# Kernel tuning notes

Hardware: AMD Instinct MI355X
Metric: run time of the kernel (lower is better)

Reference implementation:

```python
import jax, jax.numpy as jnp
import numpy as np

I, H, O, K = 64, 512, 3, 6  # input, hidden, output classes, num heads


def setup_inputs() -> dict:
    key = jax.random.key(0)
    ks = jax.random.split(key, 8)
    B, T = 256, 512
    s = 0.05
    return {
        "x": jax.random.normal(ks[0], (B, T, I), dtype=jnp.float32),
        "W_ih": jax.random.normal(ks[1], (4 * H, I), dtype=jnp.float32) * s,
        "W_hh": jax.random.normal(ks[2], (4 * H, H), dtype=jnp.float32) * s,
        "b_ih": jax.random.normal(ks[3], (4 * H,), dtype=jnp.float32) * s,
        "b_hh": jax.random.normal(ks[4], (4 * H,), dtype=jnp.float32) * s,
        "W_heads": jax.random.normal(ks[5], (K, O, H), dtype=jnp.float32) * s,
        "b_heads": jax.random.normal(ks[6], (K, O), dtype=jnp.float32) * s,
    }


def _lstm_last_h(x, W_ih, W_hh, b_ih, b_hh):
    # x: [B, T, I]; returns final hidden state h_T: [B, H]
    B = x.shape[0]
    h0 = jnp.zeros((B, H), dtype=x.dtype)
    c0 = jnp.zeros((B, H), dtype=x.dtype)
    # precompute input projections for all timesteps: [T, B, 4H]
    x_proj = jnp.einsum('bti,gi->tbg', x, W_ih) + b_ih + b_hh

    def step(carry, xp_t):
        h, c = carry
        gates = xp_t + h @ W_hh.T  # [B, 4H]
        i_g, f_g, g_g, o_g = jnp.split(gates, 4, axis=-1)  # PyTorch gate order i,f,g,o
        i_g = jax.nn.sigmoid(i_g)
        f_g = jax.nn.sigmoid(f_g)
        g_g = jnp.tanh(g_g)
        o_g = jax.nn.sigmoid(o_g)
        c = f_g * c + i_g * g_g
        h = o_g * jnp.tanh(c)
        return (h, c), None

    (h_T, _), _ = jax.lax.scan(step, (h0, c0), x_proj)
    return h_T


def reference(x, W_ih, W_hh, b_ih, b_hh, W_heads, b_heads):
    h_T = _lstm_last_h(x, W_ih, W_hh, b_ih, b_hh)  # [B, H]
    # six parallel linear heads on last hidden state -> stacked [6, B, O]
    out = jnp.einsum('koh,bh->kbo', W_heads, h_T) + b_heads[:, None, :]
    return out
```

## Files before the change

### kernel.cpp

```cpp
#include <hip/hip_runtime.h>
#include <hip/hip_bf16.h>
#include <cstdint>

#define TSTEPS 512
#define BATCH  256
#define HID    512
#define INP    64
#define NGRP   16
#define GROWS  16
#define NSL    16
#define NWG    256
#define KTH    16
#define RING   8

typedef __attribute__((ext_vector_type(8))) short short8;
typedef __attribute__((ext_vector_type(4))) float f32x4;
typedef __attribute__((ext_vector_type(2))) float f32x2;
typedef __attribute__((ext_vector_type(2))) unsigned long long ull2;

#define HB_OFF    0
#define HT_OFF    (RING*BATCH*HID*2)
#define FLAGS_OFF (HT_OFF + BATCH*HID*4)
#define FLAGS_SZ  (NGRP*NSL*64)
#define CNT_OFF   (FLAGS_OFF + FLAGS_SZ)
#define ZERO2_SZ  (FLAGS_SZ + 64)

__device__ __forceinline__ unsigned cvtpk(float a, float b) {
    unsigned r;
    asm("v_cvt_pk_bf16_f32 %0, %1, %2" : "=v"(r) : "v"(a), "v"(b));
    return r;
}
__device__ __forceinline__ short8 pack8(float4 a0, float4 a1) {
    uint4 u = { cvtpk(a0.x, a0.y), cvtpk(a0.z, a0.w),
                cvtpk(a1.x, a1.y), cvtpk(a1.z, a1.w) };
    return __builtin_bit_cast(short8, u);
}
__device__ __forceinline__ float sigm(float x)  { return 1.0f/(1.0f + __expf(-x)); }
__device__ __forceinline__ float tanhf_(float x){ return 2.0f/(1.0f + __expf(-2.0f*x)) - 1.0f; }

__global__ void __launch_bounds__(256, 1)
lstm_persist(const float* __restrict__ x,   const float* __restrict__ Wih,
             const float* __restrict__ Whh, const float* __restrict__ bih,
             const float* __restrict__ bhh, const float* __restrict__ Whead,
             const float* __restrict__ bhead, float* __restrict__ out,
             char* __restrict__ ws)
{
    extern __shared__ char lds[];
    const int tid  = threadIdx.x;
    const int lane = tid & 63;
    const int wv   = tid >> 6;
    const int l15  = lane & 15, lq = lane >> 4;

    unsigned short* hb = (unsigned short*)(ws + HB_OFF);
    float* hT  = (float*)(ws + HT_OFF);
    unsigned* flags = (unsigned*)(ws + FLAGS_OFF);
    int* cnt   = (int*)(ws + CNT_OFF);

    int* org = (int*)(lds + 131056);
    if (tid == 0) {
        unsigned xcd;
        asm volatile("s_getreg_b32 %0, hwreg(HW_REG_XCC_ID)" : "=s"(xcd));
        xcd &= 7u;
        int slot = __hip_atomic_fetch_add(&cnt[xcd], 1, __ATOMIC_RELAXED, __HIP_MEMORY_SCOPE_AGENT) & 31;
        org[0] = (int)xcd * 2 + (slot >> 4);
        org[1] = slot & 15;
    }
    __syncthreads();
    const int g  = org[0];
    const int sl = org[1];
    const int hb8 = sl*32 + wv*8;

    short8 whh[KTH][2];
    #pragma unroll
    for (int kt = 0; kt < KTH; ++kt)
        #pragma unroll
        for (int m = 0; m < 2; ++m) {
            int grow = (l15 & 3)*HID + hb8 + m*4 + (l15 >> 2);
            const float4* p = (const float4*)(Whh + (size_t)grow*HID + kt*32 + lq*8);
            whh[kt][m] = pack8(p[0], p[1]);
        }
    short8 wihf[2][2];
    #pragma unroll
    for (int kt = 0; kt < 2; ++kt)
        #pragma unroll
        for (int m = 0; m < 2; ++m) {
            int grow = (l15 & 3)*HID + hb8 + m*4 + (l15 >> 2);
            const float4* p = (const float4*)(Wih + (size_t)grow*INP + kt*32 + lq*8);
            wihf[kt][m] = pack8(p[0], p[1]);
        }
    f32x4 bias[2];
    #pragma unroll
    for (int m = 0; m < 2; ++m)
        #pragma unroll
        for (int r = 0; r < 4; ++r) {
            int hc = hb8 + m*4 + lq;
            bias[m][r] = bih[r*HID + hc] + bhh[r*HID + hc];
        }

    unsigned short* hgrp = hb + (size_t)g*GROWS*HID;
    float*          hTg  = hT + (size_t)g*GROWS*HID;

    unsigned* flg  = flags + (size_t)g*NSL*16;
    unsigned* fpub = flg + sl*16;
    const unsigned* fpoll = flg + (4*wv + lq)*16;

    const int skt = tid >> 4, sr = tid & 15;
    char* swp = lds + skt*1024 + sr*16;
    const char* srp = lds + lane*16;

    const float* xrow = x + ((size_t)(g*GROWS + l15)*TSTEPS)*INP + lq*8;

    f32x2 cst = {0.f, 0.f};

    float4 xv0 = *(const float4*)(xrow);
    float4 xv1 = *(const float4*)(xrow + 4);
    float4 xv2 = *(const float4*)(xrow + 32);
    float4 xv3 = *(const float4*)(xrow + 36);

    #pragma clang loop unroll(disable)
    for (int t = 0; t < TSTEPS; ++t) {
        short8 bfx0 = pack8(xv0, xv1);
        short8 bfx1 = pack8(xv2, xv3);
        f32x4 a0 = bias[0], a1 = bias[1];
        f32x4 b0 = {0.f,0.f,0.f,0.f}, b1 = {0.f,0.f,0.f,0.f};
        a0 = __builtin_amdgcn_mfma_f32_16x16x32_bf16(wihf[0][0], bfx0, a0, 0, 0, 0);
        a1 = __builtin_amdgcn_mfma_f32_16x16x32_bf16(wihf[0][1], bfx0, a1, 0, 0, 0);
        b0 = __builtin_amdgcn_mfma_f32_16x16x32_bf16(wihf[1][0], bfx1, b0, 0, 0, 0);
        b1 = __builtin_amdgcn_mfma_f32_16x16x32_bf16(wihf[1][1], bfx1, b1, 0, 0, 0);
        __builtin_amdgcn_sched_barrier(0);

        if (t) {
            if (l15 == 0) {
                while (__hip_atomic_load(fpoll, __ATOMIC_RELAXED, __HIP_MEMORY_SCOPE_AGENT)
                       < (unsigned)t) {}
            }
            __builtin_amdgcn_sched_barrier(0);
            asm volatile("" ::: "memory");
        }

        {
            const char* gsrc = (const char*)(hgrp + (size_t)(t & (RING-1))*BATCH*HID)
                               + sr*1024 + skt*64;
            ull2 w0 = *(const ull2*)(gsrc);
            ull2 w1 = *(const ull2*)(gsrc + 16);
            ull2 w2 = *(const ull2*)(gsrc + 32);
            ull2 w3 = *(const ull2*)(gsrc + 48);
            *(ull2*)(swp      ) = w0;
            *(ull2*)(swp + 256) = w1;
            *(ull2*)(swp + 512) = w2;
            *(ull2*)(swp + 768) = w3;
        }
        __syncthreads();

        if (t + 1 < TSTEPS) {
            const float* xn = xrow + (size_t)(t+1)*INP;
            xv0 = *(const float4*)(xn);      xv1 = *(const float4*)(xn + 4);
            xv2 = *(const float4*)(xn + 32); xv3 = *(const float4*)(xn + 36);
        }

        #pragma unroll
        for (int k2 = 0; k2 < 8; ++k2) {
            short8 be = *(const short8*)(srp + (2*k2  )*1024);
            short8 bo = *(const short8*)(srp + (2*k2+1)*1024);
            a0 = __builtin_amdgcn_mfma_f32_16x16x32_bf16(whh[2*k2  ][0], be, a0, 0, 0, 0);
            a1 = __builtin_amdgcn_mfma_f32_16x16x32_bf16(whh[2*k2  ][1], be, a1, 0, 0, 0);
            b0 = __builtin_amdgcn_mfma_f32_16x16x32_bf16(whh[2*k2+1][0], bo, b0, 0, 0, 0);
            b1 = __builtin_amdgcn_mfma_f32_16x16x32_bf16(whh[2*k2+1][1], bo, b1, 0, 0, 0);
        }
        f32x4 acc0 = a0 + b0;
        f32x4 acc1 = a1 + b1;

        unsigned short* hbw = hgrp + (size_t)((t+1) & (RING-1))*BATCH*HID;
        #pragma unroll
        for (int m = 0; m < 2; ++m) {
            f32x4 A = m ? acc1 : acc0;
            float c = sigm(A[1])*cst[m] + sigm(A[0])*tanhf_(A[2]);
            cst[m] = c;
            float h = sigm(A[3])*tanhf_(c);
            int idx = l15*HID + hb8 + m*4 + lq;
            hbw[idx] = (unsigned short)(cvtpk(h, h) & 0xffffu);
            if (t == TSTEPS-1) hTg[idx] = h;
        }
        __syncthreads();
        if (tid == 0)
            __hip_atomic_store(fpub, (unsigned)(t+1),
                               __ATOMIC_RELAXED, __HIP_MEMORY_SCOPE_AGENT);
    }

    if (sl == 0) {
        {
            unsigned v;
            do {
                v = (lane < NSL)
                    ? __hip_atomic_load(flg + lane*16, __ATOMIC_RELAXED, __HIP_MEMORY_SCOPE_AGENT)
                    : (unsigned)TSTEPS;
            } while (!__all(v >= (unsigned)TSTEPS));
            asm volatile("" ::: "memory");
        }
        __syncthreads();
        {
            const float4* gp = (const float4*)((const char*)hTg + tid*128);
            float4* wp = (float4*)(lds + tid*128);
            #pragma unroll
            for (int j = 0; j < 8; ++j) wp[j] = gp[j];
        }
        __syncthreads();
        const float* hsm = (const float*)lds;
        for (int idx = tid; idx < 6*GROWS*3; idx += 256) {
            int k = idx / (GROWS*3), rem = idx % (GROWS*3);
            int row = rem / 3, o = rem % 3;
            const float* wp = Whead + ((size_t)k*3 + o)*HID;
            const float* hp = hsm + row*HID;
            float s = 0.f;
            for (int hh = 0; hh < HID; hh += 4) {
                float4 hv = *(const float4*)(hp + hh);
                float4 wv2 = *(const float4*)(wp + hh);
                s += hv.x*wv2.x + hv.y*wv2.y + hv.z*wv2.z + hv.w*wv2.w;
            }
            out[((size_t)k*BATCH + g*GROWS + row)*3 + o] = s + bhead[k*3 + o];
        }
    }
}

extern "C" void kernel_launch(void* const* d_in, const int* in_sizes, int n_in,
                              void* d_out, int out_size, void* d_ws, size_t ws_size,
                              hipStream_t stream) {
    (void)in_sizes; (void)n_in; (void)out_size; (void)ws_size;
    const float* x     = (const float*)d_in[0];
    const float* Wih   = (const float*)d_in[1];
    const float* Whh   = (const float*)d_in[2];
    const float* bih   = (const float*)d_in[3];
    const float* bhh   = (const float*)d_in[4];
    const float* Whead = (const float*)d_in[5];
    const float* bhead = (const float*)d_in[6];
    char* ws = (char*)d_ws;

    (void)hipFuncSetAttribute((const void*)lstm_persist,
                              hipFuncAttributeMaxDynamicSharedMemorySize, 131072);

    (void)hipMemsetAsync(ws + HB_OFF, 0, BATCH*HID*2, stream);
    (void)hipMemsetAsync(ws + FLAGS_OFF, 0, ZERO2_SZ, stream);

    hipLaunchKernelGGL(lstm_persist, dim3(NWG), dim3(256), 131072, stream,
                       x, Wih, Whh, bih, bhh, Whead, bhead, (float*)d_out, ws);
}
```

Measured before the change: 1.006 ms.

## Pack adjacent hidden columns per lane and overlap x prefetch with barrier

Remaps the weight rows so each lane owns two adjacent hidden columns, allowing the bf16 hidden-state write to become a single packed 32-bit store and the final fp32 write a vector store. Moves the next-timestep x prefetch after the gate computation and replaces __syncthreads with a manual vmcnt(4) wait plus s_barrier, so the x loads stay in flight across the barrier. This is meant to cut store count and per-step latency on the serial recurrence. It risks memory-ordering errors if the hand-written waitcnt doesn't cover the h stores before the flag publish.

```diff
diff --git a/kernel.cpp b/kernel.cpp
--- a/kernel.cpp
+++ b/kernel.cpp
@@ -75,7 +75,7 @@
     for (int kt = 0; kt < KTH; ++kt)
         #pragma unroll
         for (int m = 0; m < 2; ++m) {
-            int grow = (l15 & 3)*HID + hb8 + m*4 + (l15 >> 2);
+            int grow = (l15 & 3)*HID + hb8 + 2*(l15 >> 2) + m;
             const float4* p = (const float4*)(Whh + (size_t)grow*HID + kt*32 + lq*8);
             whh[kt][m] = pack8(p[0], p[1]);
         }
@@ -84,7 +84,7 @@
     for (int kt = 0; kt < 2; ++kt)
         #pragma unroll
         for (int m = 0; m < 2; ++m) {
-            int grow = (l15 & 3)*HID + hb8 + m*4 + (l15 >> 2);
+            int grow = (l15 & 3)*HID + hb8 + 2*(l15 >> 2) + m;
             const float4* p = (const float4*)(Wih + (size_t)grow*INP + kt*32 + lq*8);
             wihf[kt][m] = pack8(p[0], p[1]);
         }
@@ -93,7 +93,7 @@
     for (int m = 0; m < 2; ++m)
         #pragma unroll
         for (int r = 0; r < 4; ++r) {
-            int hc = hb8 + m*4 + lq;
+            int hc = hb8 + 2*lq + m;
             bias[m][r] = bih[r*HID + hc] + bhh[r*HID + hc];
         }
 
@@ -152,12 +152,6 @@
         }
         __syncthreads();
 
-        if (t + 1 < TSTEPS) {
-            const float* xn = xrow + (size_t)(t+1)*INP;
-            xv0 = *(const float4*)(xn);      xv1 = *(const float4*)(xn + 4);
-            xv2 = *(const float4*)(xn + 32); xv3 = *(const float4*)(xn + 36);
-        }
-
         #pragma unroll
         for (int k2 = 0; k2 < 8; ++k2) {
             short8 be = *(const short8*)(srp + (2*k2  )*1024);
@@ -171,17 +165,30 @@
         f32x4 acc1 = a1 + b1;
 
         unsigned short* hbw = hgrp + (size_t)((t+1) & (RING-1))*BATCH*HID;
-        #pragma unroll
-        for (int m = 0; m < 2; ++m) {
-            f32x4 A = m ? acc1 : acc0;
-            float c = sigm(A[1])*cst[m] + sigm(A[0])*tanhf_(A[2]);
-            cst[m] = c;
-            float h = sigm(A[3])*tanhf_(c);
-            int idx = l15*HID + hb8 + m*4 + lq;
-            hbw[idx] = (unsigned short)(cvtpk(h, h) & 0xffffu);
-            if (t == TSTEPS-1) hTg[idx] = h;
-        }
-        __syncthreads();
+        float c0 = sigm(acc0[1])*cst[0] + sigm(acc0[0])*tanhf_(acc0[2]);
+        float c1 = sigm(acc1[1])*cst[1] + sigm(acc1[0])*tanhf_(acc1[2]);
+        cst[0] = c0; cst[1] = c1;
+        float h0 = sigm(acc0[3])*tanhf_(c0);
+        float h1 = sigm(acc1[3])*tanhf_(c1);
+        const int cidx = l15*HID + hb8 + 2*lq;
+        *(unsigned*)((char*)hbw + (size_t)cidx*2) = cvtpk(h0, h1);
+        if (t == TSTEPS-1) {
+            f32x2 hv2 = {h0, h1};
+            *(f32x2*)(hTg + cidx) = hv2;
+        }
+        __builtin_amdgcn_sched_barrier(0);
+
+        {
+            int tn = (t + 1 < TSTEPS) ? t + 1 : t;
+            const float* xn = xrow + (size_t)tn*INP;
+            xv0 = *(const float4*)(xn);      xv1 = *(const float4*)(xn + 4);
+            xv2 = *(const float4*)(xn + 32); xv3 = *(const float4*)(xn + 36);
+        }
+        __builtin_amdgcn_sched_barrier(0);
+        asm volatile("s_waitcnt vmcnt(4)" ::: "memory");
+        __builtin_amdgcn_sched_barrier(0);
+        __builtin_amdgcn_s_barrier();
+        __builtin_amdgcn_sched_barrier(0);
         if (tid == 0)
             __hip_atomic_store(fpub, (unsigned)(t+1),
                                __ATOMIC_RELAXED, __HIP_MEMORY_SCOPE_AGENT);
```

New measurement: 1.241 ms. 23.4% more time.
